# Kernel optimization log

Measured on AMD Instinct MI355X. Metric: run time of the kernel, lower is better.

## Reference

```python
import jax, jax.numpy as jnp
import numpy as np

B, T, E, HEAD_S = 8, 4096, 2048, 128


def setup_inputs() -> dict:
    key = jax.random.key(0)
    kx, kq, kk, kv = jax.random.split(key, 4)
    x = jax.random.normal(kx, (B, T, E), dtype=jnp.float32)
    # Linear weights initialized ~N(0, 0.02) as in the repo's _init_weights
    Wq = jax.random.normal(kq, (E, HEAD_S), dtype=jnp.float32) * 0.02
    Wk = jax.random.normal(kk, (E, HEAD_S), dtype=jnp.float32) * 0.02
    Wv = jax.random.normal(kv, (E, HEAD_S), dtype=jnp.float32) * 0.02
    return {"x": x, "Wq": Wq, "Wk": Wk, "Wv": Wv}


def reference(x, Wq, Wk, Wv):
    # x: [B,T,E]; W*: [E,D]
    q = jnp.einsum('bte,ed->btd', x, Wq)
    k = jnp.einsum('bte,ed->btd', x, Wk)
    v = jnp.einsum('bte,ed->btd', x, Wv)
    scale = k.shape[-1] ** -0.5
    # scores: [B, T(query), S(key)]
    wei = jnp.einsum('btd,bsd->bts', q, k) * scale
    Tn = x.shape[1]
    causal = jnp.tril(jnp.ones((Tn, Tn), dtype=bool))  # [T,S], True where allowed
    wei = jnp.where(causal[None, :, :], wei, -jnp.inf)
    # NOTE: original code applies softmax over dim=1 (the QUERY axis) —
    # faithful reproduction of that behavior. Each key-column j has finite
    # entries for queries i >= j, so no NaNs arise.
    wei = jax.nn.softmax(wei, axis=1)
    # dropout is identity in eval mode
    out = jnp.einsum('bts,bsd->btd', wei, v)  # [B,T,D]
    return out
```

## Files before the change

### kernel.cpp

```cpp
#include <hip/hip_runtime.h>
#include <hip/hip_bf16.h>

#define TLEN 4096
#define EDIM 2048
#define DDIM 128
#define BSZ  8
#define NT   32
#define MROWS (BSZ*TLEN)
#define NSLOT 528

typedef unsigned short u16;
typedef __attribute__((ext_vector_type(8))) short bf16x8;
typedef __attribute__((ext_vector_type(4))) float f32x4;

#define C1F (0.08838834764831845f * 1.4426950408889634f)

__device__ __forceinline__ u16 f2bf(float f) {
  unsigned u = __builtin_bit_cast(unsigned, f);
  u += 0x7FFFu + ((u >> 16) & 1u);
  return (u16)(u >> 16);
}
__device__ __forceinline__ float bf2f(u16 h) {
  unsigned u = ((unsigned)h) << 16;
  return __builtin_bit_cast(float, u);
}

__device__ __forceinline__ void async_ld16(const void* g, void* lds) {
  __builtin_amdgcn_global_load_lds(
      (const __attribute__((address_space(1))) unsigned int*)(g),
      (__attribute__((address_space(3))) unsigned int*)(lds), 16, 0, 0);
}

__device__ __forceinline__ int swz16(int row, int chunk) {
  return row * 256 + ((chunk ^ (row & 15)) << 4);
}
__device__ __forceinline__ int swz8(int row, int chunk) {
  return row * 128 + ((chunk ^ (row & 7)) << 4);
}

__global__ __launch_bounds__(256) void zero_f32(float* __restrict__ out,
                                                float* __restrict__ denom) {
  size_t i = (size_t)blockIdx.x * 256 + threadIdx.x;
  float4 z = {0.f, 0.f, 0.f, 0.f};
  if (i < (size_t)MROWS * DDIM / 4) ((float4*)out)[i] = z;
  if (i < (size_t)BSZ * TLEN / 4) ((float4*)denom)[i] = z;
}

__global__ __launch_bounds__(256) void prep_w(const float* __restrict__ Wq,
                                              const float* __restrict__ Wk,
                                              const float* __restrict__ Wv,
                                              u16* __restrict__ Wt) {
  int g = blockIdx.x * 256 + threadIdx.x;
  int w = g >> 15;
  int rem = g & 32767;
  int n = rem >> 8;
  int k0 = (rem & 255) * 8;
  const float* W = (w == 0) ? Wq : (w == 1) ? Wk : Wv;
  unsigned pk[4];
  for (int i = 0; i < 4; ++i) {
    u16 lo = f2bf(W[(size_t)(k0 + 2 * i) * DDIM + n]);
    u16 hi = f2bf(W[(size_t)(k0 + 2 * i + 1) * DDIM + n]);
    pk[i] = (unsigned)lo | ((unsigned)hi << 16);
  }
  uint4 v; v.x = pk[0]; v.y = pk[1]; v.z = pk[2]; v.w = pk[3];
  *(uint4*)(Wt + ((size_t)(w * DDIM + n) * EDIM + k0)) = v;
}

__global__ __launch_bounds__(512, 2) void qkv_gemm(const float* __restrict__ x,
                                                   const u16* __restrict__ Wt,
                                                   u16* __restrict__ qkvb) {
  __shared__ u16 As[128 * 64];
  __shared__ u16 Bs[384 * 64];
  const int tid = threadIdx.x, lane = tid & 63, wave = tid >> 6;
  const int quad = lane >> 4, l15 = lane & 15;
  const int m0 = blockIdx.x * 128;
  const int wm = wave & 1, wn = wave >> 1;

  const f32x4 zero = {0.f, 0.f, 0.f, 0.f};
  f32x4 acc[4][6];
  for (int mi = 0; mi < 4; ++mi)
    for (int ni = 0; ni < 6; ++ni) acc[mi][ni] = zero;

  int arow[4], af4[4];
  for (int i = 0; i < 4; ++i) {
    int c = i * 512 + tid;
    arow[i] = c >> 4;
    af4[i] = c & 15;
  }
  float4 ap[4];
#define LOADA(KT)                                                            \
  for (int i = 0; i < 4; ++i)                                                \
    ap[i] = *(const float4*)(x + (size_t)(m0 + arow[i]) * EDIM + (KT)*64 +   \
                             af4[i] * 4);
  LOADA(0)

  for (int kt = 0; kt < EDIM / 64; ++kt) {
    __syncthreads();
    for (int i = 0; i < 4; ++i) {
      uint2 pk;
      pk.x = (unsigned)f2bf(ap[i].x) | ((unsigned)f2bf(ap[i].y) << 16);
      pk.y = (unsigned)f2bf(ap[i].z) | ((unsigned)f2bf(ap[i].w) << 16);
      *(uint2*)((char*)As + swz8(arow[i], af4[i] >> 1) + (af4[i] & 1) * 8) = pk;
    }
    {
      const int k0 = kt * 64;
      for (int e = 0; e < 6; ++e) {
        int rb = (wave * 6 + e) * 8;
        int r = rb + (lane >> 3);
        int c = (lane & 7) ^ (r & 7);
        async_ld16((const char*)(Wt + (size_t)r * EDIM + k0) + c * 16,
                   (char*)Bs + rb * 128);
      }
    }
    __builtin_amdgcn_s_waitcnt(0);
    __syncthreads();
    if (kt + 1 < EDIM / 64) { LOADA(kt + 1) }
    for (int ks = 0; ks < 2; ++ks) {
      const int ch = ks * 4 + quad;
      bf16x8 afr[4], bfr[6];
      for (int mi = 0; mi < 4; ++mi)
        afr[mi] = *(const bf16x8*)((char*)As + swz8(wm * 64 + mi * 16 + l15, ch));
      for (int ni = 0; ni < 6; ++ni)
        bfr[ni] = *(const bf16x8*)((char*)Bs + swz8(wn * 96 + ni * 16 + l15, ch));
      for (int mi = 0; mi < 4; ++mi)
        for (int ni = 0; ni < 6; ++ni)
          acc[mi][ni] = __builtin_amdgcn_mfma_f32_16x16x32_bf16(afr[mi], bfr[ni], acc[mi][ni], 0, 0, 0);
    }
  }
#undef LOADA
  for (int mi = 0; mi < 4; ++mi)
    for (int ni = 0; ni < 6; ++ni) {
      int n = wn * 96 + ni * 16 + l15;
      u16* ob = qkvb + (size_t)(n >> 7) * MROWS * DDIM;
      int nc = n & 127;
      for (int r = 0; r < 4; ++r) {
        int row = m0 + wm * 64 + mi * 16 + quad * 4 + r;
        ob[(size_t)row * DDIM + nc] = f2bf(acc[mi][ni][r]);
      }
    }
}

__global__ __launch_bounds__(256) void score_k(const u16* __restrict__ qb,
                                               const u16* __restrict__ kb,
                                               char* __restrict__ Epack,
                                               float* __restrict__ denom) {
  __shared__ u16 Kbuf[128 * 128];
  __shared__ u16 Qbuf[128 * 128];
  const int tid = threadIdx.x, lane = tid & 63, wave = tid >> 6;
  const int quad = lane >> 4, l15 = lane & 15;
  const int jt = blockIdx.x, ic = blockIdx.y, b = blockIdx.z;
  const int len = NT - jt;
  const int cl = (len + 3) >> 2;
  if (ic * cl >= len) return;
  const int beg = jt + ic * cl;
  const int end = (beg + cl < NT) ? beg + cl : NT;
  const int j0 = jt * 128;

  {
    const char* gk = (const char*)kb + (size_t)(b * TLEN + j0) * 256;
    for (int e = 0; e < 8; ++e) {
      int rb = (wave * 8 + e) * 4;
      int r = rb + (lane >> 4);
      int c = l15 ^ (r & 15);
      async_ld16(gk + r * 256 + c * 16, (char*)Kbuf + rb * 256);
    }
  }
  __builtin_amdgcn_s_waitcnt(0);
  __syncthreads();

  float csum[8];
  for (int ni = 0; ni < 8; ++ni) csum[ni] = 0.f;
  const f32x4 zero = {0.f, 0.f, 0.f, 0.f};

  for (int it = beg; it < end; ++it) {
    const int i0 = it * 128;
    {
      const char* gq = (const char*)qb + (size_t)(b * TLEN + i0) * 256;
      for (int e = 0; e < 8; ++e) {
        int rb = (wave * 8 + e) * 4;
        int r = rb + (lane >> 4);
        int c = l15 ^ (r & 15);
        async_ld16(gq + r * 256 + c * 16, (char*)Qbuf + rb * 256);
      }
    }
    __builtin_amdgcn_s_waitcnt(0);

    f32x4 accS[2][8];
    for (int mi = 0; mi < 2; ++mi)
      for (int ni = 0; ni < 8; ++ni) accS[mi][ni] = zero;
    for (int ks = 0; ks < 4; ++ks) {
      const int ch = ks * 4 + quad;
      bf16x8 afr[2], kfr[8];
      for (int mi = 0; mi < 2; ++mi)
        afr[mi] = *(const bf16x8*)((char*)Qbuf + swz16(wave * 32 + mi * 16 + l15, ch));
      for (int ni = 0; ni < 8; ++ni)
        kfr[ni] = *(const bf16x8*)((char*)Kbuf + swz16(ni * 16 + l15, ch));
      for (int mi = 0; mi < 2; ++mi)
        for (int ni = 0; ni < 8; ++ni)
          accS[mi][ni] = __builtin_amdgcn_mfma_f32_16x16x32_bf16(afr[mi], kfr[ni], accS[mi][ni], 0, 0, 0);
    }
    const bool diag = (it == jt);
    for (int mi = 0; mi < 2; ++mi)
      for (int ni = 0; ni < 8; ++ni)
        for (int r = 0; r < 4; ++r) {
          float e = exp2f(C1F * accS[mi][ni][r]);
          int rrow = wave * 32 + mi * 16 + quad * 4 + r;
          int jl = ni * 16 + l15;
          if (diag && (i0 + rrow) < (j0 + jl)) e = 0.f;
          csum[ni] += e;
          *(u16*)((char*)Qbuf + swz16(rrow, jl >> 3) + (jl & 7) * 2) = f2bf(e);
        }
    char* eslot = Epack + (((size_t)b * NSLOT + (size_t)it * (it + 1) / 2 + jt) << 15);
    for (int e = 0; e < 8; ++e) {
      int row = wave * 32 + e * 4 + (lane >> 4);
      bf16x8 v = *(const bf16x8*)((char*)Qbuf + swz16(row, l15));
      *(bf16x8*)(eslot + row * 256 + l15 * 16) = v;
    }
  }
  for (int ni = 0; ni < 8; ++ni) {
    csum[ni] += __shfl_xor(csum[ni], 16, 64);
    csum[ni] += __shfl_xor(csum[ni], 32, 64);
  }
  __syncthreads();
  float* red = (float*)Kbuf;
  if (lane < 16)
    for (int ni = 0; ni < 8; ++ni)
      red[wave * 128 + ni * 16 + lane] = csum[ni];
  __syncthreads();
  if (tid < 128)
    atomicAdd(&denom[(size_t)b * TLEN + j0 + tid],
              red[tid] + red[128 + tid] + red[256 + tid] + red[384 + tid]);
}

__global__ __launch_bounds__(256) void vscale_t(const u16* __restrict__ vb,
                                                const float* __restrict__ denom,
                                                u16* __restrict__ vbT) {
  __shared__ u16 tile[128 * 136];
  const int tid = threadIdx.x;
  const int t0 = blockIdx.x * 128, b = blockIdx.y;
  for (int i = 0; i < 8; ++i) {
    int c = tid + i * 256;
    int tl = c >> 4, ch = c & 15;
    float rd = 1.0f / denom[(size_t)b * TLEN + t0 + tl];
    uint4 v = *(const uint4*)(vb + ((size_t)(b * TLEN + t0 + tl) * DDIM + ch * 8));
    unsigned w[4] = {v.x, v.y, v.z, v.w};
    unsigned o[4];
    for (int j = 0; j < 4; ++j) {
      float lo = bf2f((u16)w[j]) * rd;
      float hi = bf2f((u16)(w[j] >> 16)) * rd;
      o[j] = (unsigned)f2bf(lo) | ((unsigned)f2bf(hi) << 16);
    }
    uint4 ov; ov.x = o[0]; ov.y = o[1]; ov.z = o[2]; ov.w = o[3];
    *(uint4*)(tile + tl * 136 + ch * 8) = ov;
  }
  __syncthreads();
  for (int i = 0; i < 8; ++i) {
    int c = tid + i * 256;
    int d = c >> 4, ch = c & 15;
    unsigned pk[4];
    for (int j = 0; j < 4; ++j) {
      u16 lo = tile[(ch * 8 + 2 * j) * 136 + d];
      u16 hi = tile[(ch * 8 + 2 * j + 1) * 136 + d];
      pk[j] = (unsigned)lo | ((unsigned)hi << 16);
    }
    uint4 v; v.x = pk[0]; v.y = pk[1]; v.z = pk[2]; v.w = pk[3];
    *(uint4*)(vbT + ((size_t)(b * DDIM + d) * TLEN + t0 + ch * 8)) = v;
  }
}

__global__ __launch_bounds__(256, 3) void pv_k(const char* __restrict__ Epack,
                                               const u16* __restrict__ vbT,
                                               float* __restrict__ out) {
  __shared__ u16 Es[128 * 64];
  __shared__ u16 Vs[128 * 64];
  const int tid = threadIdx.x, lane = tid & 63, wave = tid >> 6;
  const int quad = lane >> 4, l15 = lane & 15;
  const int it = blockIdx.x, jc = blockIdx.y, b = blockIdx.z;
  const int nsub = 2 * (it + 1);
  const int sBeg = jc * 16;
  if (sBeg >= nsub) return;
  const int sEnd = (sBeg + 16 < nsub) ? sBeg + 16 : nsub;
  const int i0 = it * 128;
  const int wm = wave & 1, wn = wave >> 1;

  const f32x4 zero = {0.f, 0.f, 0.f, 0.f};
  f32x4 accO[4][4];
  for (int mi = 0; mi < 4; ++mi)
    for (int ni = 0; ni < 4; ++ni) accO[mi][ni] = zero;

  const size_t triBase = ((size_t)b * NSLOT + (size_t)it * (it + 1) / 2) << 15;
  const char* vbase = (const char*)vbT + (size_t)b * DDIM * TLEN * 2;

  for (int s = sBeg; s < sEnd; ++s) {
    const int jt = s >> 1, h = s & 1;
    __syncthreads();
    {
      const char* eb = Epack + triBase + ((size_t)jt << 15) + h * 128;
      const char* vb2 = vbase + s * 128;
      for (int e = 0; e < 4; ++e) {
        int rb = (wave * 4 + e) * 8;
        int r = rb + (lane >> 3);
        int c = (lane & 7) ^ (r & 7);
        async_ld16(eb + r * 256 + c * 16, (char*)Es + rb * 128);
        async_ld16(vb2 + (size_t)r * (TLEN * 2) + c * 16, (char*)Vs + rb * 128);
      }
    }
    __builtin_amdgcn_s_waitcnt(0);
    __syncthreads();
    for (int ks = 0; ks < 2; ++ks) {
      const int ch = ks * 4 + quad;
      bf16x8 afr[4], bfr[4];
      for (int mi = 0; mi < 4; ++mi)
        afr[mi] = *(const bf16x8*)((char*)Es + swz8(wm * 64 + mi * 16 + l15, ch));
      for (int ni = 0; ni < 4; ++ni)
        bfr[ni] = *(const bf16x8*)((char*)Vs + swz8(wn * 64 + ni * 16 + l15, ch));
      for (int mi = 0; mi < 4; ++mi)
        for (int ni = 0; ni < 4; ++ni)
          accO[mi][ni] = __builtin_amdgcn_mfma_f32_16x16x32_bf16(afr[mi], bfr[ni], accO[mi][ni], 0, 0, 0);
    }
  }
  const bool excl = (it < 8);
  for (int mi = 0; mi < 4; ++mi)
    for (int ni = 0; ni < 4; ++ni) {
      int d = wn * 64 + ni * 16 + l15;
      for (int r = 0; r < 4; ++r) {
        int row = i0 + wm * 64 + mi * 16 + quad * 4 + r;
        float* dst = &out[((size_t)b * TLEN + row) * DDIM + d];
        if (excl) *dst = accO[mi][ni][r];
        else atomicAdd(dst, accO[mi][ni][r]);
      }
    }
}

extern "C" void kernel_launch(void* const* d_in, const int* in_sizes, int n_in,
                              void* d_out, int out_size, void* d_ws, size_t ws_size,
                              hipStream_t stream) {
  const float* x  = (const float*)d_in[0];
  const float* Wq = (const float*)d_in[1];
  const float* Wk = (const float*)d_in[2];
  const float* Wv = (const float*)d_in[3];
  float* out = (float*)d_out;

  u16* qb  = (u16*)d_ws;
  u16* kb  = qb  + (size_t)MROWS * DDIM;
  u16* vb  = kb  + (size_t)MROWS * DDIM;
  u16* vbT = vb  + (size_t)MROWS * DDIM;
  u16* Wt  = vbT + (size_t)MROWS * DDIM;
  float* denom = (float*)(Wt + (size_t)3 * DDIM * EDIM);
  char* Epack = (char*)(denom + (size_t)BSZ * TLEN);

  hipLaunchKernelGGL(zero_f32, dim3(4096), dim3(256), 0, stream, out, denom);
  hipLaunchKernelGGL(prep_w, dim3(384), dim3(256), 0, stream, Wq, Wk, Wv, Wt);
  hipLaunchKernelGGL(qkv_gemm, dim3(256), dim3(512), 0, stream, x, Wt, qb);
  hipLaunchKernelGGL(score_k, dim3(NT, 4, BSZ), dim3(256), 0, stream, qb, kb, Epack, denom);
  hipLaunchKernelGGL(vscale_t, dim3(NT, BSZ), dim3(256), 0, stream, vb, denom, vbT);
  hipLaunchKernelGGL(pv_k, dim3(NT, 4, BSZ), dim3(256), 0, stream, Epack, vbT, out);
}
```

Measured before the change: 625.8 us.

## Split QKV GEMM per weight matrix and double-buffer LDS tiles

The QKV projection kernel now launches a 3x256 grid, so each block computes a 128x128 tile for a single weight (Q, K or V) instead of a 128x384 tile. The main loop double-buffers the A and B LDS tiles. The next tile's async weight loads and the fp32-to-bf16 conversion of x are issued before the current tile's MFMAs, with explicit waitcnt and barriers. This gives more blocks and higher occupancy (launch bounds 4) and overlaps memory with compute, but x is now read and converted three times, once per weight block.

```diff
diff --git a/kernel.cpp b/kernel.cpp
--- a/kernel.cpp
+++ b/kernel.cpp
@@ -66,20 +66,23 @@
   *(uint4*)(Wt + ((size_t)(w * DDIM + n) * EDIM + k0)) = v;
 }
 
-__global__ __launch_bounds__(512, 2) void qkv_gemm(const float* __restrict__ x,
+__global__ __launch_bounds__(512, 4) void qkv_gemm(const float* __restrict__ x,
                                                    const u16* __restrict__ Wt,
                                                    u16* __restrict__ qkvb) {
-  __shared__ u16 As[128 * 64];
-  __shared__ u16 Bs[384 * 64];
+  __shared__ u16 As[2][128 * 64];
+  __shared__ u16 Bs[2][128 * 64];
   const int tid = threadIdx.x, lane = tid & 63, wave = tid >> 6;
   const int quad = lane >> 4, l15 = lane & 15;
-  const int m0 = blockIdx.x * 128;
+  const int w = blockIdx.x;
+  const int m0 = blockIdx.y * 128;
   const int wm = wave & 1, wn = wave >> 1;
+  const int NK = EDIM / 64;
+  const u16* Wtw = Wt + (size_t)w * DDIM * EDIM;
 
   const f32x4 zero = {0.f, 0.f, 0.f, 0.f};
-  f32x4 acc[4][6];
+  f32x4 acc[4][2];
   for (int mi = 0; mi < 4; ++mi)
-    for (int ni = 0; ni < 6; ++ni) acc[mi][ni] = zero;
+    for (int ni = 0; ni < 2; ++ni) acc[mi][ni] = zero;
 
   int arow[4], af4[4];
   for (int i = 0; i < 4; ++i) {
@@ -88,54 +91,79 @@
     af4[i] = c & 15;
   }
   float4 ap[4];
+
 #define LOADA(KT)                                                            \
   for (int i = 0; i < 4; ++i)                                                \
     ap[i] = *(const float4*)(x + (size_t)(m0 + arow[i]) * EDIM + (KT)*64 +   \
                              af4[i] * 4);
+
+#define ISSUEB(KT, BUF)                                                      \
+  {                                                                          \
+    const int k0_ = (KT)*64;                                                 \
+    for (int e = 0; e < 2; ++e) {                                            \
+      int rb = (wave * 2 + e) * 8;                                           \
+      int r = rb + (lane >> 3);                                              \
+      int c = (lane & 7) ^ (r & 7);                                          \
+      async_ld16((const char*)(Wtw + (size_t)r * EDIM + k0_) + c * 16,       \
+                 (char*)(BUF) + rb * 128);                                   \
+    }                                                                        \
+  }
+
+#define CVTA(BUF)                                                            \
+  for (int i = 0; i < 4; ++i) {                                              \
+    uint2 pk;                                                                \
+    pk.x = (unsigned)f2bf(ap[i].x) | ((unsigned)f2bf(ap[i].y) << 16);        \
+    pk.y = (unsigned)f2bf(ap[i].z) | ((unsigned)f2bf(ap[i].w) << 16);        \
+    *(uint2*)((char*)(BUF) + swz8(arow[i], af4[i] >> 1) + (af4[i] & 1) * 8) = pk; \
+  }
+
   LOADA(0)
-
-  for (int kt = 0; kt < EDIM / 64; ++kt) {
-    __syncthreads();
-    for (int i = 0; i < 4; ++i) {
-      uint2 pk;
-      pk.x = (unsigned)f2bf(ap[i].x) | ((unsigned)f2bf(ap[i].y) << 16);
-      pk.y = (unsigned)f2bf(ap[i].z) | ((unsigned)f2bf(ap[i].w) << 16);
-      *(uint2*)((char*)As + swz8(arow[i], af4[i] >> 1) + (af4[i] & 1) * 8) = pk;
-    }
-    {
-      const int k0 = kt * 64;
-      for (int e = 0; e < 6; ++e) {
-        int rb = (wave * 6 + e) * 8;
-        int r = rb + (lane >> 3);
-        int c = (lane & 7) ^ (r & 7);
-        async_ld16((const char*)(Wt + (size_t)r * EDIM + k0) + c * 16,
-                   (char*)Bs + rb * 128);
-      }
-    }
-    __builtin_amdgcn_s_waitcnt(0);
-    __syncthreads();
-    if (kt + 1 < EDIM / 64) { LOADA(kt + 1) }
+  ISSUEB(0, Bs[0])
+  asm volatile("s_waitcnt vmcnt(2)" ::: "memory");
+  CVTA(As[0])
+  LOADA(1)
+  asm volatile("s_waitcnt vmcnt(4) lgkmcnt(0)" ::: "memory");
+  __builtin_amdgcn_s_barrier();
+
+  for (int kt = 0; kt < NK; ++kt) {
+    const int cur = kt & 1, nxt = cur ^ 1;
+    if (kt + 1 < NK) {
+      ISSUEB(kt + 1, Bs[nxt])
+      asm volatile("s_waitcnt vmcnt(2)" ::: "memory");
+      CVTA(As[nxt])
+      if (kt + 2 < NK) { LOADA(kt + 2) }
+    }
     for (int ks = 0; ks < 2; ++ks) {
       const int ch = ks * 4 + quad;
-      bf16x8 afr[4], bfr[6];
+      bf16x8 afr[4], bfr[2];
       for (int mi = 0; mi < 4; ++mi)
-        afr[mi] = *(const bf16x8*)((char*)As + swz8(wm * 64 + mi * 16 + l15, ch));
-      for (int ni = 0; ni < 6; ++ni)
-        bfr[ni] = *(const bf16x8*)((char*)Bs + swz8(wn * 96 + ni * 16 + l15, ch));
+        afr[mi] = *(const bf16x8*)((char*)As[cur] + swz8(wm * 64 + mi * 16 + l15, ch));
+      for (int ni = 0; ni < 2; ++ni)
+        bfr[ni] = *(const bf16x8*)((char*)Bs[cur] + swz8(wn * 32 + ni * 16 + l15, ch));
       for (int mi = 0; mi < 4; ++mi)
-        for (int ni = 0; ni < 6; ++ni)
+        for (int ni = 0; ni < 2; ++ni)
           acc[mi][ni] = __builtin_amdgcn_mfma_f32_16x16x32_bf16(afr[mi], bfr[ni], acc[mi][ni], 0, 0, 0);
     }
+    if (kt + 1 < NK) {
+      if (kt + 2 < NK) {
+        asm volatile("s_waitcnt vmcnt(4) lgkmcnt(0)" ::: "memory");
+      } else {
+        asm volatile("s_waitcnt vmcnt(0) lgkmcnt(0)" ::: "memory");
+      }
+      __builtin_amdgcn_sched_barrier(0);
+      __builtin_amdgcn_s_barrier();
+    }
   }
 #undef LOADA
+#undef ISSUEB
+#undef CVTA
+  u16* ob = qkvb + (size_t)w * MROWS * DDIM;
   for (int mi = 0; mi < 4; ++mi)
-    for (int ni = 0; ni < 6; ++ni) {
-      int n = wn * 96 + ni * 16 + l15;
-      u16* ob = qkvb + (size_t)(n >> 7) * MROWS * DDIM;
-      int nc = n & 127;
+    for (int ni = 0; ni < 2; ++ni) {
+      int n = wn * 32 + ni * 16 + l15;
       for (int r = 0; r < 4; ++r) {
         int row = m0 + wm * 64 + mi * 16 + quad * 4 + r;
-        ob[(size_t)row * DDIM + nc] = f2bf(acc[mi][ni][r]);
+        ob[(size_t)row * DDIM + n] = f2bf(acc[mi][ni][r]);
       }
     }
 }
@@ -351,7 +379,7 @@
 
   hipLaunchKernelGGL(zero_f32, dim3(4096), dim3(256), 0, stream, out, denom);
   hipLaunchKernelGGL(prep_w, dim3(384), dim3(256), 0, stream, Wq, Wk, Wv, Wt);
-  hipLaunchKernelGGL(qkv_gemm, dim3(256), dim3(512), 0, stream, x, Wt, qb);
+  hipLaunchKernelGGL(qkv_gemm, dim3(3, 256), dim3(512), 0, stream, x, Wt, qb);
   hipLaunchKernelGGL(score_k, dim3(NT, 4, BSZ), dim3(256), 0, stream, qb, kb, Epack, denom);
   hipLaunchKernelGGL(vscale_t, dim3(NT, BSZ), dim3(256), 0, stream, vb, denom, vbT);
   hipLaunchKernelGGL(pv_k, dim3(NT, 4, BSZ), dim3(256), 0, stream, Epack, vbT, out);
```

New measurement: 621.9 us. About the same (-0.6%).

## Double-buffer QKV GEMM LDS tiles with K=32 steps and async prefetch

Applied to the files above, without the earlier changes.

The QKV projection GEMM now uses two LDS buffers with K-step 32 instead of a single buffer with K-step 64. It issues the async global-to-LDS loads of W and the fp32 loads of x one or two steps ahead, using explicit vmcnt waits and one barrier per iteration. A new swizzle handles the 64-byte rows. The goal is to overlap memory latency with MFMA work and drop the full waitcnt(0) plus double syncthreads, at the cost of more iterations and delicate hand-counted wait logic.

```diff
diff --git a/kernel.cpp b/kernel.cpp
--- a/kernel.cpp
+++ b/kernel.cpp
@@ -36,6 +36,9 @@
 }
 __device__ __forceinline__ int swz8(int row, int chunk) {
   return row * 128 + ((chunk ^ (row & 7)) << 4);
+}
+__device__ __forceinline__ int swz4(int row, int chunk) {
+  return (row >> 1) * 128 + ((((row & 1) << 2) | ((chunk ^ (row >> 1)) & 3)) << 4);
 }
 
 __global__ __launch_bounds__(256) void zero_f32(float* __restrict__ out,
@@ -69,65 +72,96 @@
 __global__ __launch_bounds__(512, 2) void qkv_gemm(const float* __restrict__ x,
                                                    const u16* __restrict__ Wt,
                                                    u16* __restrict__ qkvb) {
-  __shared__ u16 As[128 * 64];
-  __shared__ u16 Bs[384 * 64];
+  __shared__ u16 As[2][128 * 32];
+  __shared__ u16 Bs[2][384 * 32];
   const int tid = threadIdx.x, lane = tid & 63, wave = tid >> 6;
   const int quad = lane >> 4, l15 = lane & 15;
   const int m0 = blockIdx.x * 128;
   const int wm = wave & 1, wn = wave >> 1;
+  const int NK = EDIM / 32;
 
   const f32x4 zero = {0.f, 0.f, 0.f, 0.f};
   f32x4 acc[4][6];
   for (int mi = 0; mi < 4; ++mi)
     for (int ni = 0; ni < 6; ++ni) acc[mi][ni] = zero;
 
-  int arow[4], af4[4];
-  for (int i = 0; i < 4; ++i) {
+  int arow[2], af4[2];
+  for (int i = 0; i < 2; ++i) {
     int c = i * 512 + tid;
-    arow[i] = c >> 4;
-    af4[i] = c & 15;
-  }
-  float4 ap[4];
+    arow[i] = c >> 3;
+    af4[i] = c & 7;
+  }
+  float4 ap[2];
+
+  int brow[3], bch[3];
+  for (int e = 0; e < 3; ++e) {
+    int rb = (wave * 3 + e) * 16;
+    int g16 = rb * 4 + lane;
+    int p = g16 >> 3, s = g16 & 7;
+    brow[e] = 2 * p + (s >> 2);
+    bch[e] = (s & 3) ^ (p & 3);
+  }
+
 #define LOADA(KT)                                                            \
-  for (int i = 0; i < 4; ++i)                                                \
-    ap[i] = *(const float4*)(x + (size_t)(m0 + arow[i]) * EDIM + (KT)*64 +   \
+  for (int i = 0; i < 2; ++i)                                                \
+    ap[i] = *(const float4*)(x + (size_t)(m0 + arow[i]) * EDIM + (KT)*32 +   \
                              af4[i] * 4);
+
+#define ISSUEB(KT, BUF)                                                      \
+  for (int e = 0; e < 3; ++e) {                                              \
+    int rb = (wave * 3 + e) * 16;                                            \
+    async_ld16((const char*)Wt + (size_t)brow[e] * (EDIM * 2) + (KT)*64 +    \
+                   bch[e] * 16,                                              \
+               (char*)(BUF) + rb * 64);                                      \
+  }
+
+#define CVTA(BUF)                                                            \
+  for (int i = 0; i < 2; ++i) {                                              \
+    uint2 pk;                                                                \
+    pk.x = (unsigned)f2bf(ap[i].x) | ((unsigned)f2bf(ap[i].y) << 16);        \
+    pk.y = (unsigned)f2bf(ap[i].z) | ((unsigned)f2bf(ap[i].w) << 16);        \
+    *(uint2*)((char*)(BUF) + swz4(arow[i], af4[i] >> 1) + (af4[i] & 1) * 8) = pk; \
+  }
+
   LOADA(0)
-
-  for (int kt = 0; kt < EDIM / 64; ++kt) {
-    __syncthreads();
-    for (int i = 0; i < 4; ++i) {
-      uint2 pk;
-      pk.x = (unsigned)f2bf(ap[i].x) | ((unsigned)f2bf(ap[i].y) << 16);
-      pk.y = (unsigned)f2bf(ap[i].z) | ((unsigned)f2bf(ap[i].w) << 16);
-      *(uint2*)((char*)As + swz8(arow[i], af4[i] >> 1) + (af4[i] & 1) * 8) = pk;
+  ISSUEB(0, Bs[0])
+  asm volatile("s_waitcnt vmcnt(3)" ::: "memory");
+  CVTA(As[0])
+  LOADA(1)
+  asm volatile("s_waitcnt vmcnt(2) lgkmcnt(0)" ::: "memory");
+  __builtin_amdgcn_s_barrier();
+
+  for (int kt = 0; kt < NK; ++kt) {
+    const int cur = kt & 1, nxt = cur ^ 1;
+    if (kt + 1 < NK) {
+      ISSUEB(kt + 1, Bs[nxt])
+      asm volatile("s_waitcnt vmcnt(3)" ::: "memory");
+      CVTA(As[nxt])
+      if (kt + 2 < NK) { LOADA(kt + 2) }
     }
     {
-      const int k0 = kt * 64;
-      for (int e = 0; e < 6; ++e) {
-        int rb = (wave * 6 + e) * 8;
-        int r = rb + (lane >> 3);
-        int c = (lane & 7) ^ (r & 7);
-        async_ld16((const char*)(Wt + (size_t)r * EDIM + k0) + c * 16,
-                   (char*)Bs + rb * 128);
-      }
-    }
-    __builtin_amdgcn_s_waitcnt(0);
-    __syncthreads();
-    if (kt + 1 < EDIM / 64) { LOADA(kt + 1) }
-    for (int ks = 0; ks < 2; ++ks) {
-      const int ch = ks * 4 + quad;
       bf16x8 afr[4], bfr[6];
       for (int mi = 0; mi < 4; ++mi)
-        afr[mi] = *(const bf16x8*)((char*)As + swz8(wm * 64 + mi * 16 + l15, ch));
+        afr[mi] = *(const bf16x8*)((char*)As[cur] + swz4(wm * 64 + mi * 16 + l15, quad));
       for (int ni = 0; ni < 6; ++ni)
-        bfr[ni] = *(const bf16x8*)((char*)Bs + swz8(wn * 96 + ni * 16 + l15, ch));
+        bfr[ni] = *(const bf16x8*)((char*)Bs[cur] + swz4(wn * 96 + ni * 16 + l15, quad));
       for (int mi = 0; mi < 4; ++mi)
         for (int ni = 0; ni < 6; ++ni)
           acc[mi][ni] = __builtin_amdgcn_mfma_f32_16x16x32_bf16(afr[mi], bfr[ni], acc[mi][ni], 0, 0, 0);
     }
+    if (kt + 1 < NK) {
+      if (kt + 2 < NK) {
+        asm volatile("s_waitcnt vmcnt(2) lgkmcnt(0)" ::: "memory");
+      } else {
+        asm volatile("s_waitcnt vmcnt(0) lgkmcnt(0)" ::: "memory");
+      }
+      __builtin_amdgcn_sched_barrier(0);
+      __builtin_amdgcn_s_barrier();
+    }
   }
 #undef LOADA
+#undef ISSUEB
+#undef CVTA
   for (int mi = 0; mi < 4; ++mi)
     for (int ni = 0; ni < 6; ++ni) {
       int n = wn * 96 + ni * 16 + l15;
```

After: 605.4 us. -3.3%, faster.
